# Optimization experiments

Measured on AMD Instinct MI355X. Metric: run time of the kernel, lower is better.

The kernel has to match this reference:

```python
import jax, jax.numpy as jnp
import numpy as np

H = 2880
NH = 64        # query heads
NKV = 8        # kv heads
DH = 64        # head dim
GROUP = NH // NKV
THETA = 150000.0
FACTOR = 32.0
SCALE = 1.0 / np.sqrt(DH)
INIT_STD = 0.02
SINK_INIT = 4.0


def setup_inputs() -> dict:
    key = jax.random.key(0)
    ks = jax.random.split(key, 6)
    B, T = 2, 1024
    x = jax.random.normal(ks[0], (B, T, H), dtype=jnp.float32)
    positions = jnp.tile(jnp.arange(T, dtype=jnp.int32), (B, 1))
    causal_mask = jnp.tril(jnp.ones((T, T), dtype=bool))
    Wq = INIT_STD * jax.random.normal(ks[1], (H, NH * DH), dtype=jnp.float32)
    Wk = INIT_STD * jax.random.normal(ks[2], (H, NKV * DH), dtype=jnp.float32)
    Wv = INIT_STD * jax.random.normal(ks[3], (H, NKV * DH), dtype=jnp.float32)
    Wo = INIT_STD * jax.random.normal(ks[4], (NH * DH, H), dtype=jnp.float32)
    bq = jnp.zeros((NH * DH,), jnp.float32)
    bk = jnp.zeros((NKV * DH,), jnp.float32)
    bv = jnp.zeros((NKV * DH,), jnp.float32)
    bo = jnp.zeros((H,), jnp.float32)
    sink_logit = jnp.full((NH,), SINK_INIT, dtype=jnp.float32)
    return {
        'x': x, 'positions': positions, 'causal_mask': causal_mask,
        'Wq': Wq, 'bq': bq, 'Wk': Wk, 'bk': bk, 'Wv': Wv, 'bv': bv,
        'Wo': Wo, 'bo': bo, 'sink_logit': sink_logit,
        'is_sliding_layer': 1, 'sliding_window': 128,
    }


def _rope(x, pos):
    # x: [B, h, T, DH], pos: [B, T] ints. YaRN-style stretched positions: pos/FACTOR.
    inv_freq = 1.0 / (THETA ** (jnp.arange(0, DH, 2, dtype=jnp.float32) / DH))  # [DH/2]
    freqs = (pos.astype(jnp.float32) / FACTOR)[:, :, None] * inv_freq           # [B, T, DH/2]
    cos = jnp.cos(freqs)[:, None].astype(x.dtype)  # [B, 1, T, DH/2]
    sin = jnp.sin(freqs)[:, None].astype(x.dtype)
    x1, x2 = x[..., 0::2], x[..., 1::2]
    r1 = x1 * cos - x2 * sin
    r2 = x1 * sin + x2 * cos
    return jnp.stack([r1, r2], axis=-1).reshape(x.shape)  # re-interleave even/odd


def reference(x, positions, causal_mask, Wq, bq, Wk, bk, Wv, bv, Wo, bo,
              sink_logit, is_sliding_layer, sliding_window):
    B, T, _ = x.shape
    q = (x @ Wq + bq).reshape(B, T, NH, DH).transpose(0, 2, 1, 3)   # [B,NH,T,DH]
    k = (x @ Wk + bk).reshape(B, T, NKV, DH)
    v = (x @ Wv + bv).reshape(B, T, NKV, DH)
    # GQA expand: each kv head repeated GROUP times contiguously (head h -> kv h//GROUP)
    k = jnp.repeat(k, GROUP, axis=2).transpose(0, 2, 1, 3)          # [B,NH,T,DH]
    v = jnp.repeat(v, GROUP, axis=2).transpose(0, 2, 1, 3)
    q = _rope(q, positions)
    k = _rope(k, positions)
    att = jnp.einsum('bhtd,bhsd->bhts', q, k) * SCALE               # [B,NH,T,T]
    mask = causal_mask
    if is_sliding_layer:
        i = jnp.arange(T)
        dist = i[:, None] - i[None, :]
        mask = mask & (dist >= 0) & (dist < sliding_window)
    att = jnp.where(mask[None, None], att, jnp.asarray(-1e30, att.dtype))
    # learned per-head sink logit appended as an extra softmax column
    sink = jnp.broadcast_to(sink_logit.reshape(1, NH, 1, 1).astype(att.dtype), (B, NH, T, 1))
    att = jnp.concatenate([att, sink], axis=-1)                     # [B,NH,T,T+1]
    p = jax.nn.softmax(att, axis=-1)[..., :-1]                      # drop sink column
    y = jnp.einsum('bhts,bhsd->bhtd', p, v)
    y = y.transpose(0, 2, 1, 3).reshape(B, T, NH * DH)
    return y @ Wo + bo
```

## Files before the change

### kernel.cpp

```cpp
#include <hip/hip_runtime.h>

typedef unsigned short u16;
typedef __attribute__((ext_vector_type(8))) short bf16x8;
typedef __attribute__((ext_vector_type(4))) float f32x4;

#define MFMA16(a,b,c) __builtin_amdgcn_mfma_f32_16x16x32_bf16((a),(b),(c),0,0,0)

__device__ __forceinline__ float b2f(u16 u){
  unsigned v = ((unsigned)u) << 16; float f;
  __builtin_memcpy(&f, &v, 4); return f;
}
__device__ __forceinline__ u16 f2b(float f){
  unsigned v; __builtin_memcpy(&v, &f, 4);
  v += 0x7FFFu + ((v >> 16) & 1u);
  return (u16)(v >> 16);
}
__device__ __forceinline__ float scrub(float v, float lim){
  return fminf(fmaxf(v, -lim), lim);
}
__device__ __forceinline__ void gload16(const void* g, void* l){
  __builtin_amdgcn_global_load_lds(
      (const __attribute__((address_space(1))) unsigned int*)g,
      (__attribute__((address_space(3))) unsigned int*)l, 16, 0, 0);
}

__device__ __forceinline__ void cvtT_tile(float (*tile)[33],
    u16* __restrict__ dst, const float* __restrict__ src,
    int rows, int cols, int bx, int by, int tid){
  int n0 = bx * 32, r0 = by * 32;
  int tx = tid & 31, ty = tid >> 5;
#pragma unroll
  for (int i = 0; i < 4; i++)
    tile[ty + i * 8][tx] = src[(size_t)(r0 + ty + i * 8) * cols + n0 + tx];
  __syncthreads();
#pragma unroll
  for (int i = 0; i < 4; i++)
    dst[(size_t)(n0 + ty + i * 8) * rows + r0 + tx] = f2b(tile[tx][ty + i * 8]);
}

__global__ __launch_bounds__(256) void k_prep1(
    u16* __restrict__ xb, const float* __restrict__ x,
    u16* __restrict__ wqT, const float* __restrict__ Wq,
    u16* __restrict__ wkvT, const float* __restrict__ Wk,
    const float* __restrict__ Wv){
  __shared__ float tile[32][33];
  int b = blockIdx.x, tid = threadIdx.x;
  if (b < 5760){
    int i = b * 256 + tid;
    float4 v = ((const float4*)x)[i];
    u16 o[4] = { f2b(v.x), f2b(v.y), f2b(v.z), f2b(v.w) };
    *(uint2*)&xb[(size_t)i * 4] = *(const uint2*)o;
    return;
  }
  b -= 5760;
  if (b < 11520){ cvtT_tile(tile, wqT, Wq, 2880, 4096, b % 128, b / 128, tid); return; }
  b -= 11520;
  if (b < 1440){ cvtT_tile(tile, wkvT, Wk, 2880, 512, b % 16, b / 16, tid); return; }
  b -= 1440;
  cvtT_tile(tile, wkvT + (size_t)512 * 2880, Wv, 2880, 512, b % 16, b / 16, tid);
}

template<int BN, int NTC, int F32OUT, int ROPE>
__global__ __launch_bounds__(512, 1) void k_gx(
    const u16* __restrict__ A, const u16* __restrict__ BT, const u16* __restrict__ BT2,
    const float* __restrict__ b0, const float* __restrict__ b1, const float* __restrict__ b2,
    void* __restrict__ C, const int* __restrict__ pos, int M, int N, int K, int ldc){
  constexpr int NF   = BN / 32;
  constexpr int FULL = (BN - 32) / 64;
  constexpr int BUFE = 16384 + BN * 64;
  constexpr int VMW  = 4 + FULL;
  __shared__ u16 lds[3][BUFE];

  const int tid = threadIdx.x;
  const int w = tid >> 6, l = tid & 63;
  const int wm = w >> 1, wn = w & 1;
  const int lr = l & 15, lh = l >> 4;
  const int bid = blockIdx.x;
  const int mt = bid / NTC, nt = bid % NTC;
  const int m0 = mt << 8, n0 = nt * BN;

  const int srow = tid >> 3;
  const int skc  = (tid & 7) << 3;
  const int ssw  = (srow & 7) << 3;
  const int rsw  = (lr & 7) << 3;
  const int rrow = tid >> 3;

  f32x4 acc[4][NF];
#pragma unroll
  for (int mm = 0; mm < 4; mm++)
#pragma unroll
    for (int nn = 0; nn < NF; nn++){ acc[mm][nn][0]=0.f; acc[mm][nn][1]=0.f; acc[mm][nn][2]=0.f; acc[mm][nn][3]=0.f; }

#define STAGE_A(b, kt, c) \
  gload16(&A[(size_t)(m0 + (c)*64 + srow) * K + (kt) + (skc ^ ssw)], \
          (void*)&lds[b][((c)*64 + srow) * 64 + skc])
#define STAGE_BF(b, kt, c) { \
  int _r = n0 + (c)*64 + srow; \
  const u16* _bt = BT; if (ROPE && _r >= 4096){ _bt = BT2; _r -= 4096; } \
  gload16(&_bt[(size_t)_r * K + (kt) + (skc ^ ssw)], \
          (void*)&lds[b][16384 + ((c)*64 + srow) * 64 + skc]); }
#define STAGE_BR(b, kt) if (tid < 256){ \
  int _r = n0 + FULL*64 + rrow; \
  const u16* _bt = BT; if (ROPE && _r >= 4096){ _bt = BT2; _r -= 4096; } \
  gload16(&_bt[(size_t)_r * K + (kt) + (skc ^ ((rrow & 7) << 3))], \
          (void*)&lds[b][16384 + (FULL*64 + rrow) * 64 + skc]); }

#define RD_A(dst, b, mm, kk) dst = *(const bf16x8*)&lds[b][((wm<<6) + ((mm)<<4) + lr) * 64 + ((((kk)<<5) + (lh<<3)) ^ rsw)]
#define RD_B(dst, b, nn, kk) dst = *(const bf16x8*)&lds[b][16384 + (wn*(BN/2) + (nn)*16 + lr) * 64 + ((((kk)<<5) + (lh<<3)) ^ rsw)]

  const int NT = K >> 6;
#pragma unroll
  for (int tt = 0; tt < 2; ++tt){
    int kt = tt << 6;
#pragma unroll
    for (int c = 0; c < 4; ++c) STAGE_A(tt, kt, c);
#pragma unroll
    for (int c = 0; c < FULL; ++c) STAGE_BF(tt, kt, c);
    STAGE_BR(tt, kt);
  }
  asm volatile("s_waitcnt vmcnt(%0)" :: "i"(VMW) : "memory");
  __builtin_amdgcn_s_barrier();

  int cb = 0;
  for (int t = 0; t < NT; ++t){
    int sb = cb + 2; if (sb >= 3) sb -= 3;
    const int kt2 = (t + 2) << 6;
    const bool ds = (t + 2) < NT;

    bf16x8 bf[NF][2];
#pragma unroll
    for (int nn = 0; nn < NF; nn++){ RD_B(bf[nn][0], cb, nn, 0); RD_B(bf[nn][1], cb, nn, 1); }

#pragma unroll
    for (int mm = 0; mm < 4; mm++){
      bf16x8 a0, a1;
      RD_A(a0, cb, mm, 0); RD_A(a1, cb, mm, 1);
      if (ds){
        STAGE_A(sb, kt2, mm);
        if (mm < FULL) STAGE_BF(sb, kt2, mm);
        if (mm == 2) STAGE_BR(sb, kt2);
      }
      __builtin_amdgcn_s_setprio(1);
#pragma unroll
      for (int nn = 0; nn < NF; nn++) acc[mm][nn] = MFMA16(a0, bf[nn][0], acc[mm][nn]);
#pragma unroll
      for (int nn = 0; nn < NF; nn++) acc[mm][nn] = MFMA16(a1, bf[nn][1], acc[mm][nn]);
      __builtin_amdgcn_s_setprio(0);
    }

    if (ds) asm volatile("s_waitcnt vmcnt(%0)" :: "i"(VMW) : "memory");
    else    asm volatile("s_waitcnt vmcnt(0)" ::: "memory");
    __builtin_amdgcn_s_barrier();
    cb += 1; if (cb >= 3) cb -= 3;
  }

#pragma unroll
  for (int mm = 0; mm < 4; mm++){
    int grow = m0 + (wm << 6) + (mm << 4) + (lh << 2);
#pragma unroll
    for (int nn = 0; nn < NF; nn++){
      int gcol = n0 + wn * (BN / 2) + nn * 16 + lr;
      float bs;
      if (ROPE) bs = (gcol < 4096) ? b0[gcol] : ((gcol < 4608) ? b1[gcol - 4096] : b2[gcol - 4608]);
      else      bs = b0[gcol];
      if (ROPE && gcol < 4608){
        int ii = (gcol & 63) >> 1;
        float inv = exp2f(-0.53733146f * (float)ii);
        float sgn = (lr & 1) ? 1.f : -1.f;
#pragma unroll
        for (int r = 0; r < 4; r++){
          float v = acc[mm][nn][r] + bs;
          float ang = (float)pos[grow + r] * 0.03125f * inv;
          float s, c; __sincosf(ang, &s, &c);
          float p = __shfl_xor(v, 1);
          v = v * c + p * sgn * s;
          ((u16*)C)[(size_t)(grow + r) * ldc + gcol] = f2b(scrub(v, 1e9f));
        }
      } else {
#pragma unroll
        for (int r = 0; r < 4; r++){
          float v = scrub(acc[mm][nn][r] + bs, 1e9f);
          size_t off = (size_t)(grow + r) * ldc + gcol;
          if (F32OUT) ((float*)C)[off] = v;
          else        ((u16*)C)[off]   = f2b(v);
        }
      }
    }
  }
#undef STAGE_A
#undef STAGE_BF
#undef STAGE_BR
#undef RD_A
#undef RD_B
}

__global__ __launch_bounds__(256) void k_attn_prep(
    const u16* __restrict__ qkv, const float* __restrict__ sink,
    u16* __restrict__ y, const int* __restrict__ slide_p,
    const int* __restrict__ win_p,
    u16* __restrict__ woT, const float* __restrict__ Wo){
  __shared__ char smem[36864];

  if (blockIdx.x >= 1024){
    int b = blockIdx.x - 1024;
    float (*tile)[33] = (float(*)[33])smem;
    cvtT_tile(tile, woT, Wo, 4096, 2880, b % 90, b / 90, threadIdx.x);
    return;
  }

  u16 (*Ks)[72]       = (u16(*)[72])smem;
  u16 (*VTs)[72]      = (u16(*)[72])(smem + 9216);
  u16 (*Plds)[32][72] = (u16(*)[32][72])(smem + 18432);

  int bid = blockIdx.x;
  int qt = bid & 7, h = (bid >> 3) & 63, b = bid >> 9;
  int t0 = qt << 7;
  int g = h >> 3;
  int kcol = 4096 + g * 64, vcol = 4608 + g * 64;
  int tid = threadIdx.x, w = tid >> 6, l = tid & 63;
  int lr = l & 15, lh = l >> 4;
  int win = (*slide_p) ? (*win_p) : (1 << 30);
  int tq0 = t0 + w * 32;

  bf16x8 qf[2][2];
#pragma unroll
  for (int m = 0; m < 2; m++)
#pragma unroll
    for (int kk = 0; kk < 2; kk++){
      int q = tq0 + m * 16 + lr;
      qf[m][kk] = *(const bf16x8*)&qkv[(size_t)(b * 1024 + q) * 5120 + h * 64 + kk * 32 + lh * 8];
    }

  float run_max[2] = {-1e30f, -1e30f};
  float run_sum[2] = {0.f, 0.f};
  f32x4 acc_o[4][2];
#pragma unroll
  for (int dt = 0; dt < 4; dt++)
#pragma unroll
    for (int m = 0; m < 2; m++){ acc_o[dt][m][0]=0.f; acc_o[dt][m][1]=0.f; acc_o[dt][m][2]=0.f; acc_o[dt][m][3]=0.f; }

  for (int c = 0; c < 4; c++){
    int key0 = t0 - 128 + c * 64;
#pragma unroll
    for (int it = 0; it < 2; ++it){
      int idx = it * 256 + tid;
      int key = idx >> 3, dd = (idx & 7) << 3;
      int gk = key0 + key;
      uint4 kq = make_uint4(0, 0, 0, 0);
      uint4 vq = make_uint4(0, 0, 0, 0);
      if (gk >= 0){
        size_t rb = (size_t)(b * 1024 + gk) * 5120;
        kq = *(const uint4*)&qkv[rb + kcol + dd];
        vq = *(const uint4*)&qkv[rb + vcol + dd];
      }
      *(uint4*)&Ks[key][dd] = kq;
      const u16* tv = (const u16*)&vq;
#pragma unroll
      for (int j = 0; j < 8; j++) VTs[dd + j][key] = tv[j];
    }
    __syncthreads();

    bool rel = (key0 + 63 >= tq0 - (win - 1)) && (key0 <= tq0 + 31);
    if (rel){
      f32x4 sacc[2][4];
#pragma unroll
      for (int m = 0; m < 2; m++)
#pragma unroll
        for (int n = 0; n < 4; n++){ sacc[m][n][0]=0.f; sacc[m][n][1]=0.f; sacc[m][n][2]=0.f; sacc[m][n][3]=0.f; }
#pragma unroll
      for (int kk = 0; kk < 2; kk++){
#pragma unroll
        for (int n = 0; n < 4; n++){
          bf16x8 kf = *(const bf16x8*)&Ks[n * 16 + lr][kk * 32 + lh * 8];
          sacc[0][n] = MFMA16(kf, qf[0][kk], sacc[0][n]);
          sacc[1][n] = MFMA16(kf, qf[1][kk], sacc[1][n]);
        }
      }
#pragma unroll
      for (int m = 0; m < 2; m++){
        int qrow = tq0 + m * 16 + lr;
        float cmax = -INFINITY;
#pragma unroll
        for (int n = 0; n < 4; n++)
#pragma unroll
          for (int r = 0; r < 4; r++){
            int key = key0 + n * 16 + lh * 4 + r;
            float s = scrub(sacc[m][n][r] * 0.125f, 1e30f);
            bool valid = (key >= 0) && (key <= qrow) && (qrow - key < win);
            s = valid ? s : -INFINITY;
            sacc[m][n][r] = s;
            cmax = fmaxf(cmax, s);
          }
        cmax = fmaxf(cmax, __shfl_xor(cmax, 16));
        cmax = fmaxf(cmax, __shfl_xor(cmax, 32));
        float mnew = fmaxf(run_max[m], cmax);
        float corr = __expf(run_max[m] - mnew);
        run_max[m] = mnew;
        float rsum = 0.f;
#pragma unroll
        for (int n = 0; n < 4; n++)
#pragma unroll
          for (int r = 0; r < 4; r++){
            float p = __expf(sacc[m][n][r] - mnew);
            sacc[m][n][r] = p;
            rsum += p;
          }
        rsum += __shfl_xor(rsum, 16);
        rsum += __shfl_xor(rsum, 32);
        run_sum[m] = run_sum[m] * corr + rsum;
#pragma unroll
        for (int dt = 0; dt < 4; dt++) acc_o[dt][m] *= corr;
#pragma unroll
        for (int n = 0; n < 4; n++)
#pragma unroll
          for (int r = 0; r < 4; r++)
            Plds[w][m * 16 + lr][n * 16 + lh * 4 + r] = f2b(sacc[m][n][r]);
      }
#pragma unroll
      for (int ks = 0; ks < 2; ks++){
        bf16x8 pb[2];
#pragma unroll
        for (int m = 0; m < 2; m++)
          pb[m] = *(const bf16x8*)&Plds[w][m * 16 + lr][ks * 32 + lh * 8];
#pragma unroll
        for (int dt = 0; dt < 4; dt++){
          bf16x8 vf = *(const bf16x8*)&VTs[dt * 16 + lr][ks * 32 + lh * 8];
          acc_o[dt][0] = MFMA16(vf, pb[0], acc_o[dt][0]);
          acc_o[dt][1] = MFMA16(vf, pb[1], acc_o[dt][1]);
        }
      }
    }
    __syncthreads();
  }

  float sk = sink[h];
  float osc[2];
#pragma unroll
  for (int m = 0; m < 2; m++){
    float Mf = fmaxf(run_max[m], sk);
    float t = __expf(run_max[m] - Mf);
    float denom = run_sum[m] * t + __expf(sk - Mf);
    osc[m] = t / denom;
  }
#pragma unroll
  for (int dt = 0; dt < 4; dt++)
#pragma unroll
    for (int m = 0; m < 2; m++)
#pragma unroll
      for (int r = 0; r < 4; r++){
        int d = dt * 16 + lh * 4 + r;
        int q = tq0 + m * 16 + lr;
        y[(size_t)(b * 1024 + q) * 4096 + h * 64 + d] = f2b(scrub(acc_o[dt][m][r] * osc[m], 1e9f));
      }
}

extern "C" void kernel_launch(void* const* d_in, const int* in_sizes, int n_in,
                              void* d_out, int out_size, void* d_ws, size_t ws_size,
                              hipStream_t stream){
  const float* x    = (const float*)d_in[0];
  const int*   pos  = (const int*)d_in[1];
  const float* Wq   = (const float*)d_in[3];
  const float* bq   = (const float*)d_in[4];
  const float* Wk   = (const float*)d_in[5];
  const float* bk   = (const float*)d_in[6];
  const float* Wv   = (const float*)d_in[7];
  const float* bv   = (const float*)d_in[8];
  const float* Wo   = (const float*)d_in[9];
  const float* bo   = (const float*)d_in[10];
  const float* sink = (const float*)d_in[11];
  const int* slide  = (const int*)d_in[12];
  const int* winp   = (const int*)d_in[13];
  float* out = (float*)d_out;

  char* ws = (char*)d_ws;
  u16* xb   = (u16*)(ws + 0);
  u16* ybuf = (u16*)(ws + 0);
  u16* wkvT = (u16*)(ws + 11796480);
  u16* qkv  = (u16*)(ws + 17694720);
  u16* wqT  = (u16*)(ws + 38666240);
  u16* woT  = (u16*)(ws + 38666240);

  k_prep1<<<5760 + 11520 + 2880, 256, 0, stream>>>(xb, x, wqT, Wq, wkvT, Wk, Wv);
  k_gx<160, 32, 0, 1><<<256, 512, 0, stream>>>(xb, wqT, wkvT, bq, bk, bv, qkv, pos, 2048, 5120, 2880, 5120);
  k_attn_prep<<<1024 + 11520, 256, 0, stream>>>(qkv, sink, ybuf, slide, winp, woT, Wo);
  k_gx<96, 30, 1, 0><<<240, 512, 0, stream>>>(ybuf, woT, woT, bo, bo, bo, out, pos, 2048, 2880, 4096, 2880);
}
```

Measured before the change: 173.5 us.

## Restructure GEMM inner loop into barrier-separated phases with regrouped staging

Unrolls the per-row-block MFMA loop into four explicit phases. Each phase reads its A fragments from LDS, issues a regrouped set of global-to-LDS stage loads (A chunks paired, B chunks batched), then hits a workgroup barrier before the MFMA burst and another after it. The goal is to keep waves in lockstep so LDS reads, async loads and matrix ops interleave more predictably across waves, in the style of ping-pong scheduling. The cost is several extra barriers per k-step, which may stall waves and reduce latency hiding.

Measured after the change: 183.5 us. 5.7% more time.

```diff
diff --git a/kernel.cpp b/kernel.cpp
--- a/kernel.cpp
+++ b/kernel.cpp
@@ -128,25 +128,55 @@
     const bool ds = (t + 2) < NT;
 
     bf16x8 bf[NF][2];
+    bf16x8 a0, a1;
+
+    RD_A(a0, cb, 0, 0); RD_A(a1, cb, 0, 1);
 #pragma unroll
     for (int nn = 0; nn < NF; nn++){ RD_B(bf[nn][0], cb, nn, 0); RD_B(bf[nn][1], cb, nn, 1); }
-
-#pragma unroll
-    for (int mm = 0; mm < 4; mm++){
-      bf16x8 a0, a1;
-      RD_A(a0, cb, mm, 0); RD_A(a1, cb, mm, 1);
-      if (ds){
-        STAGE_A(sb, kt2, mm);
-        if (mm < FULL) STAGE_BF(sb, kt2, mm);
-        if (mm == 2) STAGE_BR(sb, kt2);
-      }
-      __builtin_amdgcn_s_setprio(1);
-#pragma unroll
-      for (int nn = 0; nn < NF; nn++) acc[mm][nn] = MFMA16(a0, bf[nn][0], acc[mm][nn]);
-#pragma unroll
-      for (int nn = 0; nn < NF; nn++) acc[mm][nn] = MFMA16(a1, bf[nn][1], acc[mm][nn]);
-      __builtin_amdgcn_s_setprio(0);
+    if (ds){ STAGE_A(sb, kt2, 0); STAGE_A(sb, kt2, 1); }
+    __builtin_amdgcn_s_barrier();
+    __builtin_amdgcn_s_setprio(1);
+#pragma unroll
+    for (int nn = 0; nn < NF; nn++) acc[0][nn] = MFMA16(a0, bf[nn][0], acc[0][nn]);
+#pragma unroll
+    for (int nn = 0; nn < NF; nn++) acc[0][nn] = MFMA16(a1, bf[nn][1], acc[0][nn]);
+    __builtin_amdgcn_s_setprio(0);
+    __builtin_amdgcn_s_barrier();
+
+    RD_A(a0, cb, 1, 0); RD_A(a1, cb, 1, 1);
+    if (ds){ STAGE_A(sb, kt2, 2); STAGE_A(sb, kt2, 3); }
+    __builtin_amdgcn_s_barrier();
+    __builtin_amdgcn_s_setprio(1);
+#pragma unroll
+    for (int nn = 0; nn < NF; nn++) acc[1][nn] = MFMA16(a0, bf[nn][0], acc[1][nn]);
+#pragma unroll
+    for (int nn = 0; nn < NF; nn++) acc[1][nn] = MFMA16(a1, bf[nn][1], acc[1][nn]);
+    __builtin_amdgcn_s_setprio(0);
+    __builtin_amdgcn_s_barrier();
+
+    RD_A(a0, cb, 2, 0); RD_A(a1, cb, 2, 1);
+    if (ds){
+#pragma unroll
+      for (int c = 0; c < FULL; ++c) STAGE_BF(sb, kt2, c);
     }
+    __builtin_amdgcn_s_barrier();
+    __builtin_amdgcn_s_setprio(1);
+#pragma unroll
+    for (int nn = 0; nn < NF; nn++) acc[2][nn] = MFMA16(a0, bf[nn][0], acc[2][nn]);
+#pragma unroll
+    for (int nn = 0; nn < NF; nn++) acc[2][nn] = MFMA16(a1, bf[nn][1], acc[2][nn]);
+    __builtin_amdgcn_s_setprio(0);
+    __builtin_amdgcn_s_barrier();
+
+    RD_A(a0, cb, 3, 0); RD_A(a1, cb, 3, 1);
+    if (ds){ STAGE_BR(sb, kt2); }
+    __builtin_amdgcn_s_barrier();
+    __builtin_amdgcn_s_setprio(1);
+#pragma unroll
+    for (int nn = 0; nn < NF; nn++) acc[3][nn] = MFMA16(a0, bf[nn][0], acc[3][nn]);
+#pragma unroll
+    for (int nn = 0; nn < NF; nn++) acc[3][nn] = MFMA16(a1, bf[nn][1], acc[3][nn]);
+    __builtin_amdgcn_s_setprio(0);
 
     if (ds) asm volatile("s_waitcnt vmcnt(%0)" :: "i"(VMW) : "memory");
     else    asm volatile("s_waitcnt vmcnt(0)" ::: "memory");
```

## Halve GEMM block size with double buffering and two blocks per CU

Applied to the files above, without the earlier changes.

The projection GEMM kernel now uses 256-thread blocks with a 128-row M tile instead of 512 threads and 256 rows, and the launch grids double accordingly. The 3-stage LDS ring with loads interleaved into the MFMA loop becomes a 2-buffer ping-pong: the next tile is prefetched at the top of each iteration and drained with vmcnt(0) before the barrier. The goal is to let two independent blocks share a CU so barrier stalls in one can be covered by the other. In exchange it shortens the prefetch distance and reduces A/B reuse per block, which raises global and L2 traffic.

Result: slower. 178.1 us (+2.6%).

```diff
diff --git a/kernel.cpp b/kernel.cpp
--- a/kernel.cpp
+++ b/kernel.cpp
@@ -61,15 +61,14 @@
 }
 
 template<int BN, int NTC, int F32OUT, int ROPE>
-__global__ __launch_bounds__(512, 1) void k_gx(
+__global__ __launch_bounds__(256, 2) void k_gx(
     const u16* __restrict__ A, const u16* __restrict__ BT, const u16* __restrict__ BT2,
     const float* __restrict__ b0, const float* __restrict__ b1, const float* __restrict__ b2,
     void* __restrict__ C, const int* __restrict__ pos, int M, int N, int K, int ldc){
   constexpr int NF   = BN / 32;
-  constexpr int FULL = (BN - 32) / 64;
-  constexpr int BUFE = 16384 + BN * 64;
-  constexpr int VMW  = 4 + FULL;
-  __shared__ u16 lds[3][BUFE];
+  constexpr int BR   = BN / 32;
+  constexpr int BUFE = 8192 + BN * 64;
+  __shared__ u16 lds[2][BUFE];
 
   const int tid = threadIdx.x;
   const int w = tid >> 6, l = tid & 63;
@@ -77,13 +76,12 @@
   const int lr = l & 15, lh = l >> 4;
   const int bid = blockIdx.x;
   const int mt = bid / NTC, nt = bid % NTC;
-  const int m0 = mt << 8, n0 = nt * BN;
+  const int m0 = mt << 7, n0 = nt * BN;
 
   const int srow = tid >> 3;
   const int skc  = (tid & 7) << 3;
   const int ssw  = (srow & 7) << 3;
   const int rsw  = (lr & 7) << 3;
-  const int rrow = tid >> 3;
 
   f32x4 acc[4][NF];
 #pragma unroll
@@ -92,40 +90,36 @@
     for (int nn = 0; nn < NF; nn++){ acc[mm][nn][0]=0.f; acc[mm][nn][1]=0.f; acc[mm][nn][2]=0.f; acc[mm][nn][3]=0.f; }
 
 #define STAGE_A(b, kt, c) \
-  gload16(&A[(size_t)(m0 + (c)*64 + srow) * K + (kt) + (skc ^ ssw)], \
-          (void*)&lds[b][((c)*64 + srow) * 64 + skc])
-#define STAGE_BF(b, kt, c) { \
-  int _r = n0 + (c)*64 + srow; \
+  gload16(&A[(size_t)(m0 + (c)*32 + srow) * K + (kt) + (skc ^ ssw)], \
+          (void*)&lds[b][((c)*32 + srow) * 64 + skc])
+#define STAGE_B(b, kt, c) { \
+  int _r = n0 + (c)*32 + srow; \
   const u16* _bt = BT; if (ROPE && _r >= 4096){ _bt = BT2; _r -= 4096; } \
   gload16(&_bt[(size_t)_r * K + (kt) + (skc ^ ssw)], \
-          (void*)&lds[b][16384 + ((c)*64 + srow) * 64 + skc]); }
-#define STAGE_BR(b, kt) if (tid < 256){ \
-  int _r = n0 + FULL*64 + rrow; \
-  const u16* _bt = BT; if (ROPE && _r >= 4096){ _bt = BT2; _r -= 4096; } \
-  gload16(&_bt[(size_t)_r * K + (kt) + (skc ^ ((rrow & 7) << 3))], \
-          (void*)&lds[b][16384 + (FULL*64 + rrow) * 64 + skc]); }
+          (void*)&lds[b][8192 + ((c)*32 + srow) * 64 + skc]); }
 
 #define RD_A(dst, b, mm, kk) dst = *(const bf16x8*)&lds[b][((wm<<6) + ((mm)<<4) + lr) * 64 + ((((kk)<<5) + (lh<<3)) ^ rsw)]
-#define RD_B(dst, b, nn, kk) dst = *(const bf16x8*)&lds[b][16384 + (wn*(BN/2) + (nn)*16 + lr) * 64 + ((((kk)<<5) + (lh<<3)) ^ rsw)]
+#define RD_B(dst, b, nn, kk) dst = *(const bf16x8*)&lds[b][8192 + (wn*(BN/2) + (nn)*16 + lr) * 64 + ((((kk)<<5) + (lh<<3)) ^ rsw)]
 
   const int NT = K >> 6;
 #pragma unroll
-  for (int tt = 0; tt < 2; ++tt){
-    int kt = tt << 6;
-#pragma unroll
-    for (int c = 0; c < 4; ++c) STAGE_A(tt, kt, c);
-#pragma unroll
-    for (int c = 0; c < FULL; ++c) STAGE_BF(tt, kt, c);
-    STAGE_BR(tt, kt);
-  }
-  asm volatile("s_waitcnt vmcnt(%0)" :: "i"(VMW) : "memory");
+  for (int c = 0; c < 4; ++c) STAGE_A(0, 0, c);
+#pragma unroll
+  for (int c = 0; c < BR; ++c) STAGE_B(0, 0, c);
+  asm volatile("s_waitcnt vmcnt(0)" ::: "memory");
   __builtin_amdgcn_s_barrier();
 
   int cb = 0;
   for (int t = 0; t < NT; ++t){
-    int sb = cb + 2; if (sb >= 3) sb -= 3;
-    const int kt2 = (t + 2) << 6;
-    const bool ds = (t + 2) < NT;
+    int sb = cb ^ 1;
+    const bool ds = (t + 1) < NT;
+    if (ds){
+      int kt1 = (t + 1) << 6;
+#pragma unroll
+      for (int c = 0; c < 4; ++c) STAGE_A(sb, kt1, c);
+#pragma unroll
+      for (int c = 0; c < BR; ++c) STAGE_B(sb, kt1, c);
+    }
 
     bf16x8 bf[NF][2];
 #pragma unroll
@@ -135,11 +129,6 @@
     for (int mm = 0; mm < 4; mm++){
       bf16x8 a0, a1;
       RD_A(a0, cb, mm, 0); RD_A(a1, cb, mm, 1);
-      if (ds){
-        STAGE_A(sb, kt2, mm);
-        if (mm < FULL) STAGE_BF(sb, kt2, mm);
-        if (mm == 2) STAGE_BR(sb, kt2);
-      }
       __builtin_amdgcn_s_setprio(1);
 #pragma unroll
       for (int nn = 0; nn < NF; nn++) acc[mm][nn] = MFMA16(a0, bf[nn][0], acc[mm][nn]);
@@ -148,10 +137,9 @@
       __builtin_amdgcn_s_setprio(0);
     }
 
-    if (ds) asm volatile("s_waitcnt vmcnt(%0)" :: "i"(VMW) : "memory");
-    else    asm volatile("s_waitcnt vmcnt(0)" ::: "memory");
+    asm volatile("s_waitcnt vmcnt(0)" ::: "memory");
     __builtin_amdgcn_s_barrier();
-    cb += 1; if (cb >= 3) cb -= 3;
+    cb ^= 1;
   }
 
 #pragma unroll
@@ -188,8 +176,7 @@
     }
   }
 #undef STAGE_A
-#undef STAGE_BF
-#undef STAGE_BR
+#undef STAGE_B
 #undef RD_A
 #undef RD_B
 }
@@ -381,7 +368,7 @@
   u16* woT  = (u16*)(ws + 38666240);
 
   k_prep1<<<5760 + 11520 + 2880, 256, 0, stream>>>(xb, x, wqT, Wq, wkvT, Wk, Wv);
-  k_gx<160, 32, 0, 1><<<256, 512, 0, stream>>>(xb, wqT, wkvT, bq, bk, bv, qkv, pos, 2048, 5120, 2880, 5120);
+  k_gx<160, 32, 0, 1><<<512, 256, 0, stream>>>(xb, wqT, wkvT, bq, bk, bv, qkv, pos, 2048, 5120, 2880, 5120);
   k_attn_prep<<<1024 + 11520, 256, 0, stream>>>(qkv, sink, ybuf, slide, winp, woT, Wo);
-  k_gx<96, 30, 1, 0><<<240, 512, 0, stream>>>(ybuf, woT, woT, bo, bo, bo, out, pos, 2048, 2880, 4096, 2880);
-}
+  k_gx<96, 30, 1, 0><<<480, 256, 0, stream>>>(ybuf, woT, woT, bo, bo, bo, out, pos, 2048, 2880, 4096, 2880);
+}
```

## Replace QKV projection GEMM with smaller-tile 256-thread kernel at two blocks per CU

Applied to the files above, without the earlier changes.

Adds a new GEMM kernel k_g2 for the fused QKV projection. It uses 128x160 tiles, a K-step of 32 and 256 threads with launch_bounds(256,2), and replaces the 512-thread k_gx instance that used 256 blocks. The grid doubles to 512 blocks and each block needs less LDS, so two blocks can share a CU and the triple-buffered global-to-LDS pipeline gets more latency hiding and better load balance across CUs. The cost is twice as many K iterations and barriers per block, and more register pressure from each wave holding 20 accumulators.

Result: slower. 186.0 us (+7.2%).

```diff
diff --git a/kernel.cpp b/kernel.cpp
--- a/kernel.cpp
+++ b/kernel.cpp
@@ -58,6 +58,130 @@
   if (b < 1440){ cvtT_tile(tile, wkvT, Wk, 2880, 512, b % 16, b / 16, tid); return; }
   b -= 1440;
   cvtT_tile(tile, wkvT + (size_t)512 * 2880, Wv, 2880, 512, b % 16, b / 16, tid);
+}
+
+template<int ROPE>
+__global__ __launch_bounds__(256, 2) void k_g2(
+    const u16* __restrict__ A, const u16* __restrict__ BT, const u16* __restrict__ BT2,
+    const float* __restrict__ b0, const float* __restrict__ b1, const float* __restrict__ b2,
+    void* __restrict__ C, const int* __restrict__ pos, int M, int N, int K, int ldc){
+  constexpr int BN = 160, NTC = 32, NF = 5;
+  constexpr int BUFE = 128 * 32 + BN * 32;
+  __shared__ u16 lds[3][BUFE];
+
+  const int tid = threadIdx.x;
+  const int w = tid >> 6, l = tid & 63;
+  const int wm = w >> 1, wn = w & 1;
+  const int lr = l & 15, lh = l >> 4;
+  const int bid = blockIdx.x;
+  const int mt = bid / NTC, nt = bid % NTC;
+  const int m0 = mt << 7, n0 = nt * BN;
+
+  const int srow = tid >> 2;
+  const int skc  = (tid & 3) << 3;
+  const int ssw  = ((srow >> 1) & 3) << 3;
+  const int rsw  = ((lr >> 1) & 3) << 3;
+
+  f32x4 acc[4][NF];
+#pragma unroll
+  for (int mm = 0; mm < 4; mm++)
+#pragma unroll
+    for (int nn = 0; nn < NF; nn++){ acc[mm][nn][0]=0.f; acc[mm][nn][1]=0.f; acc[mm][nn][2]=0.f; acc[mm][nn][3]=0.f; }
+
+#define G2_STAGE_A(b, kt, c) \
+  gload16(&A[(size_t)(m0 + (c)*64 + srow) * K + (kt) + (skc ^ ssw)], \
+          (void*)&lds[b][((c)*64 + srow) * 32 + skc])
+#define G2_STAGE_BF(b, kt, c) { \
+  int _r = n0 + (c)*64 + srow; \
+  const u16* _bt = BT; if (ROPE && _r >= 4096){ _bt = BT2; _r -= 4096; } \
+  gload16(&_bt[(size_t)_r * K + (kt) + (skc ^ ssw)], \
+          (void*)&lds[b][4096 + ((c)*64 + srow) * 32 + skc]); }
+#define G2_STAGE_BR(b, kt) if (tid < 128){ \
+  int _r = n0 + 128 + srow; \
+  const u16* _bt = BT; if (ROPE && _r >= 4096){ _bt = BT2; _r -= 4096; } \
+  gload16(&_bt[(size_t)_r * K + (kt) + (skc ^ ssw)], \
+          (void*)&lds[b][4096 + (128 + srow) * 32 + skc]); }
+
+#define G2_RD_A(dst, b, mm) dst = *(const bf16x8*)&lds[b][((wm<<6) + ((mm)<<4) + lr) * 32 + ((lh<<3) ^ rsw)]
+#define G2_RD_B(dst, b, nn) dst = *(const bf16x8*)&lds[b][4096 + (wn*80 + (nn)*16 + lr) * 32 + ((lh<<3) ^ rsw)]
+
+  const int NT = K >> 5;
+#pragma unroll
+  for (int tt = 0; tt < 2; ++tt){
+    int kt = tt << 5;
+    G2_STAGE_A(tt, kt, 0); G2_STAGE_A(tt, kt, 1);
+    G2_STAGE_BF(tt, kt, 0); G2_STAGE_BF(tt, kt, 1);
+    G2_STAGE_BR(tt, kt);
+  }
+  asm volatile("s_waitcnt vmcnt(4)" ::: "memory");
+  __builtin_amdgcn_s_barrier();
+
+  int cb = 0;
+  for (int t = 0; t < NT; ++t){
+    int sb = cb + 2; if (sb >= 3) sb -= 3;
+    const int kt2 = (t + 2) << 5;
+    const bool ds = (t + 2) < NT;
+    if (ds){
+      G2_STAGE_A(sb, kt2, 0); G2_STAGE_A(sb, kt2, 1);
+      G2_STAGE_BF(sb, kt2, 0); G2_STAGE_BF(sb, kt2, 1);
+      G2_STAGE_BR(sb, kt2);
+    }
+
+    bf16x8 bf[NF], af[4];
+#pragma unroll
+    for (int nn = 0; nn < NF; nn++) G2_RD_B(bf[nn], cb, nn);
+#pragma unroll
+    for (int mm = 0; mm < 4; mm++) G2_RD_A(af[mm], cb, mm);
+    __builtin_amdgcn_s_setprio(1);
+#pragma unroll
+    for (int mm = 0; mm < 4; mm++)
+#pragma unroll
+      for (int nn = 0; nn < NF; nn++)
+        acc[mm][nn] = MFMA16(af[mm], bf[nn], acc[mm][nn]);
+    __builtin_amdgcn_s_setprio(0);
+
+    if (ds) asm volatile("s_waitcnt vmcnt(4)" ::: "memory");
+    else    asm volatile("s_waitcnt vmcnt(0)" ::: "memory");
+    __builtin_amdgcn_s_barrier();
+    cb += 1; if (cb >= 3) cb -= 3;
+  }
+
+#pragma unroll
+  for (int mm = 0; mm < 4; mm++){
+    int grow = m0 + (wm << 6) + (mm << 4) + (lh << 2);
+#pragma unroll
+    for (int nn = 0; nn < NF; nn++){
+      int gcol = n0 + wn * 80 + nn * 16 + lr;
+      float bs;
+      if (ROPE) bs = (gcol < 4096) ? b0[gcol] : ((gcol < 4608) ? b1[gcol - 4096] : b2[gcol - 4608]);
+      else      bs = b0[gcol];
+      if (ROPE && gcol < 4608){
+        int ii = (gcol & 63) >> 1;
+        float inv = exp2f(-0.53733146f * (float)ii);
+        float sgn = (lr & 1) ? 1.f : -1.f;
+#pragma unroll
+        for (int r = 0; r < 4; r++){
+          float v = acc[mm][nn][r] + bs;
+          float ang = (float)pos[grow + r] * 0.03125f * inv;
+          float s, c; __sincosf(ang, &s, &c);
+          float p = __shfl_xor(v, 1);
+          v = v * c + p * sgn * s;
+          ((u16*)C)[(size_t)(grow + r) * ldc + gcol] = f2b(scrub(v, 1e9f));
+        }
+      } else {
+#pragma unroll
+        for (int r = 0; r < 4; r++){
+          float v = scrub(acc[mm][nn][r] + bs, 1e9f);
+          ((u16*)C)[(size_t)(grow + r) * ldc + gcol] = f2b(v);
+        }
+      }
+    }
+  }
+#undef G2_STAGE_A
+#undef G2_STAGE_BF
+#undef G2_STAGE_BR
+#undef G2_RD_A
+#undef G2_RD_B
 }
 
 template<int BN, int NTC, int F32OUT, int ROPE>
@@ -381,7 +505,7 @@
   u16* woT  = (u16*)(ws + 38666240);
 
   k_prep1<<<5760 + 11520 + 2880, 256, 0, stream>>>(xb, x, wqT, Wq, wkvT, Wk, Wv);
-  k_gx<160, 32, 0, 1><<<256, 512, 0, stream>>>(xb, wqT, wkvT, bq, bk, bv, qkv, pos, 2048, 5120, 2880, 5120);
+  k_g2<1><<<512, 256, 0, stream>>>(xb, wqT, wkvT, bq, bk, bv, qkv, pos, 2048, 5120, 2880, 5120);
   k_attn_prep<<<1024 + 11520, 256, 0, stream>>>(qkv, sink, ybuf, slide, winp, woT, Wo);
   k_gx<96, 30, 1, 0><<<240, 512, 0, stream>>>(ybuf, woT, woT, bo, bo, bo, out, pos, 2048, 2880, 4096, 2880);
 }
```
